# Kernel optimization log

Hardware: AMD Instinct MI355X
Metric: run time of the kernel (lower is better)

## Reference

```python
import jax, jax.numpy as jnp
import numpy as np

D = 2048
H = 16
HD = 128
INNER = H * HD
EPS = 1e-6


def rmsnorm(x, w):
    var = jnp.mean(x * x, axis=-1, keepdims=True)
    return x * jax.lax.rsqrt(var + EPS) * w


def setup_inputs() -> dict:
    key = jax.random.key(0)
    ks = jax.random.split(key, 10)
    B, T, N_ws, T_corr = 2, 2048, 64, 512
    scale = 1.0 / np.sqrt(D)
    return {
        "hidden_states": jax.random.normal(ks[0], (B, T, D), jnp.float32),
        "workspace": jax.random.normal(ks[1], (B, N_ws, D), jnp.float32),
        "correction_tokens": jax.random.normal(ks[2], (B, T_corr, D), jnp.float32),
        "correction_mask": jax.random.randint(ks[3], (B, T_corr), 0, 2, jnp.int32),
        "ln_q_w": jnp.ones((D,), jnp.float32),
        "ln_kv_w": jnp.ones((D,), jnp.float32),
        "Wq": jax.random.normal(ks[4], (D, INNER), jnp.float32) * scale,
        "Wk": jax.random.normal(ks[5], (D, INNER), jnp.float32) * scale,
        "Wv": jax.random.normal(ks[6], (D, INNER), jnp.float32) * scale,
        "Wo": jax.random.normal(ks[7], (INNER, D), jnp.float32) * scale,
    }


def reference(hidden_states, workspace, correction_tokens, correction_mask,
              ln_q_w, ln_kv_w, Wq, Wk, Wv, Wo):
    B, T, _ = hidden_states.shape
    N_ws = workspace.shape[1]
    # kv context = [workspace ; correction_tokens]
    kv_context = jnp.concatenate([workspace, correction_tokens], axis=1)  # (B, N_kv, D)
    N_kv = kv_context.shape[1]
    ws_mask = jnp.ones((B, N_ws), hidden_states.dtype)
    kv_mask = jnp.concatenate([ws_mask, correction_mask.astype(hidden_states.dtype)], axis=1)  # (B, N_kv)

    h = rmsnorm(hidden_states, ln_q_w)
    kv = rmsnorm(kv_context, ln_kv_w)

    q = (h @ Wq).reshape(B, T, H, HD)        # (B,T,H,hd)
    k = (kv @ Wk).reshape(B, N_kv, H, HD)
    v = (kv @ Wv).reshape(B, N_kv, H, HD)

    scores = jnp.einsum("bthd,bshd->bhts", q, k) / np.sqrt(HD)  # (B,H,T,N_kv)
    mask = (kv_mask != 0)[:, None, None, :]                      # (B,1,1,N_kv)
    scores = jnp.where(mask, scores, -jnp.inf)
    attn = jax.nn.softmax(scores, axis=-1)
    attn = jnp.nan_to_num(attn, nan=0.0)
    # dropout is identity in eval mode
    out = jnp.einsum("bhts,bshd->bthd", attn, v).reshape(B, T, INNER)
    return out @ Wo
```

## Files before the change

kernel.cpp:

```cpp
#include <hip/hip_runtime.h>
#include <hip/hip_bf16.h>
#include <math.h>

typedef __bf16 bf16;
typedef __attribute__((ext_vector_type(8))) __bf16 bf16x8;
typedef __attribute__((ext_vector_type(4))) __bf16 bf16x4;
typedef __attribute__((ext_vector_type(4))) float f32x4;

#define D_DIM 2048
#define NKV   576

__device__ inline void gld_lds16(const void* g, void* l) {
    void* gg = const_cast<void*>(g);
    __builtin_amdgcn_global_load_lds(
        (__attribute__((address_space(1))) void*)gg,
        (__attribute__((address_space(3))) void*)l, 16, 0, 0);
}

#define PH_BARRIER() do { __builtin_amdgcn_s_barrier(); asm volatile("" ::: "memory"); } while (0)
#define VMCNT(n)     asm volatile("s_waitcnt vmcnt(" #n ")" ::: "memory")

__global__ __launch_bounds__(256) void prep(
    const float* __restrict__ hidden, const float* __restrict__ wsp,
    const float* __restrict__ corr, const float* __restrict__ lnq,
    const float* __restrict__ lnkv,
    const float* __restrict__ Wq, const float* __restrict__ Wk,
    const float* __restrict__ Wv, const float* __restrict__ Wo,
    bf16* __restrict__ hb, bf16* __restrict__ kvb,
    bf16* __restrict__ WqT, bf16* __restrict__ WkvT, bf16* __restrict__ WoT)
{
    __shared__ float tl[64][65];
    __shared__ float p[4];
    const int id = blockIdx.x, t = threadIdx.x;

    if (id < 4096) {
        const int wz = id >> 10, idx = id & 1023;
        const int wy = idx >> 5, wx = idx & 31;
        const float* in; bf16* out;
        switch (wz) {
            case 0:  in = Wq; out = WqT; break;
            case 1:  in = Wk; out = WkvT; break;
            case 2:  in = Wv; out = WkvT + 2048ull * 2048; break;
            default: in = Wo; out = WoT; break;
        }
        const int r0 = wy * 64, c0 = wx * 64;
        const int tr = t >> 4, tc = (t & 15) * 4;
#pragma unroll
        for (int q = 0; q < 4; ++q) {
            const int r = tr + q * 16;
            float4 v = *(const float4*)(in + (long)(r0 + r) * 2048 + c0 + tc);
            tl[r][tc] = v.x; tl[r][tc + 1] = v.y;
            tl[r][tc + 2] = v.z; tl[r][tc + 3] = v.w;
        }
        __syncthreads();
#pragma unroll
        for (int q = 0; q < 4; ++q) {
            const int orr = tr + q * 16;
            bf16x4 o = { (bf16)tl[tc][orr], (bf16)tl[tc + 1][orr],
                         (bf16)tl[tc + 2][orr], (bf16)tl[tc + 3][orr] };
            *(bf16x4*)(out + (long)(c0 + orr) * 2048 + r0 + tc) = o;
        }
        return;
    }

    const int rr0 = id - 4096;
    const float* xr; const float* w; bf16* yr;
    if (rr0 < 4096) {
        xr = hidden + (long)rr0 * D_DIM; w = lnq; yr = hb + (long)rr0 * D_DIM;
    } else if (rr0 < 4224) {
        const int rr = rr0 - 4096;
        xr = wsp + (long)rr * D_DIM; w = lnkv;
        yr = kvb + ((long)(rr >> 6) * NKV + (rr & 63)) * D_DIM;
    } else {
        const int rr = rr0 - 4224;
        xr = corr + (long)rr * D_DIM; w = lnkv;
        yr = kvb + ((long)(rr >> 9) * NKV + 64 + (rr & 511)) * D_DIM;
    }

    float4 v0 = *(const float4*)(xr + t * 4);
    float4 v1 = *(const float4*)(xr + 1024 + t * 4);
    float ss = v0.x * v0.x + v0.y * v0.y + v0.z * v0.z + v0.w * v0.w
             + v1.x * v1.x + v1.y * v1.y + v1.z * v1.z + v1.w * v1.w;
#pragma unroll
    for (int off = 32; off; off >>= 1) ss += __shfl_xor(ss, off);
    if ((t & 63) == 0) p[t >> 6] = ss;
    __syncthreads();
    const float rs = rsqrtf((p[0] + p[1] + p[2] + p[3]) * (1.0f / 2048.0f) + 1e-6f);

    float4 w0 = *(const float4*)(w + t * 4);
    float4 w1 = *(const float4*)(w + 1024 + t * 4);
    bf16x4 o0 = { (bf16)(v0.x * rs * w0.x), (bf16)(v0.y * rs * w0.y),
                  (bf16)(v0.z * rs * w0.z), (bf16)(v0.w * rs * w0.w) };
    bf16x4 o1 = { (bf16)(v1.x * rs * w1.x), (bf16)(v1.y * rs * w1.y),
                  (bf16)(v1.z * rs * w1.z), (bf16)(v1.w * rs * w1.w) };
    *(bf16x4*)(yr + t * 4) = o0;
    *(bf16x4*)(yr + 1024 + t * 4) = o1;
}

__global__ __launch_bounds__(512, 2) void proj_all(
    const bf16* __restrict__ hb, const bf16* __restrict__ kvb,
    const bf16* __restrict__ WqT, const bf16* __restrict__ WkvT,
    bf16* __restrict__ qb, bf16* __restrict__ kb, bf16* __restrict__ vtb)
{
    __shared__ __align__(16) bf16 smem[4][16384];
    bf16* const EA = smem[0]; bf16* const EB = smem[1];
    bf16* const OA = smem[2]; bf16* const OB = smem[3];

    const int id0 = blockIdx.x;
    const int id = (id0 & 7) * 26 + (id0 >> 3);
    const bf16 *A, *B; int m0, n0; bool isQ;
    if (id < 128) {
        isQ = true;  A = hb;  B = WqT;
        m0 = (id >> 3) * 256; n0 = (id & 7) * 256;
    } else {
        const int kd = id - 128;
        isQ = false; A = kvb; B = WkvT;
        m0 = (kd >> 4) * 256; n0 = (kd & 15) * 256;
    }

    const int tid = threadIdx.x, lane = tid & 63, w = tid >> 6;
    const int wm = (w >> 2) * 128, wn = (w & 3) * 64;
    const int fr = lane & 15, fg = lane >> 4;

    f32x4 acc[8][4] = {};
    bf16x8 af[4][2], bg[4][2];

    const int aoff0 = (wm + fr) * 64 + (fg ^ (fr & 7)) * 8;
    const int boff0 = (wn + fr) * 64 + (fg ^ (fr & 7)) * 8;
    const int aoff1 = aoff0 ^ 32, boff1 = boff0 ^ 32;
    const bf16* const pAE[2] = { EA + aoff0, EA + aoff1 };
    const bf16* const pAO[2] = { OA + aoff0, OA + aoff1 };
    const bf16* const pBE[2] = { EB + boff0, EB + boff1 };
    const bf16* const pBO[2] = { OB + boff0, OB + boff1 };

    const long toff = (long)(tid >> 3) * 2048 + (((tid & 7) ^ ((tid >> 3) & 7)) * 8);
    const bf16* const gA0 = A + (long)m0 * 2048 + toff;
    const bf16* const gA1 = gA0 + 262144;
    const bf16* const gB0 = B + (long)n0 * 2048 + toff;
    const bf16* const gB1 = gB0 + 262144;
    bf16* const dT = (bf16*)smem + tid * 8;

    auto stage2 = [&](const bf16* g, int k, int dslot) {
        gld_lds16(g + k, dT + dslot);
        gld_lds16(g + 131072 + k, dT + dslot + 4096);
    };
    enum { sEA0 = 0, sEA1 = 8192, sEB0 = 16384, sEB1 = 24576,
           sOA0 = 32768, sOA1 = 40960, sOB0 = 49152, sOB1 = 57344 };

    auto load_af = [&](const bf16* const p[2], int ib) {
#pragma unroll
        for (int i = 0; i < 4; ++i)
#pragma unroll
            for (int s = 0; s < 2; ++s)
                af[i][s] = *(const bf16x8*)(p[s] + (ib + i) * 1024);
    };
    auto load_bg4 = [&](const bf16* const p[2]) {
#pragma unroll
        for (int j = 0; j < 4; ++j)
#pragma unroll
            for (int s = 0; s < 2; ++s)
                bg[j][s] = *(const bf16x8*)(p[s] + j * 1024);
    };
    auto mfma16 = [&](int ib, int jb) {
        __builtin_amdgcn_s_setprio(1);
#pragma unroll
        for (int s = 0; s < 2; ++s)
#pragma unroll
            for (int i = 0; i < 4; ++i)
#pragma unroll
                for (int j = 0; j < 2; ++j)
                    acc[ib + i][jb + j] = __builtin_amdgcn_mfma_f32_16x16x32_bf16(
                        af[i][s], bg[jb + j][s], acc[ib + i][jb + j], 0, 0, 0);
        __builtin_amdgcn_s_setprio(0);
    };

    stage2(gA0, 0, sEA0); stage2(gA1, 0, sEA1);
    stage2(gB0, 0, sEB0); stage2(gB1, 0, sEB1);
    stage2(gB0, 64, sOB0); stage2(gB1, 64, sOB1);
    stage2(gA0, 64, sOA0);
    VMCNT(6);
    PH_BARRIER();

    for (int it = 0; it < 15; ++it) {
        const int kO = it * 128 + 64, kE2 = it * 128 + 128, kO2 = it * 128 + 192;
        load_af(pAE, 0); load_bg4(pBE);
        stage2(gA1, kO, sOA1);
        PH_BARRIER(); mfma16(0, 0); PH_BARRIER();
        stage2(gB0, kE2, sEB0);
        PH_BARRIER(); mfma16(0, 2); PH_BARRIER();
        load_af(pAE, 4);
        stage2(gB1, kE2, sEB1);
        PH_BARRIER(); mfma16(4, 2); PH_BARRIER();
        stage2(gA0, kE2, sEA0);
        PH_BARRIER(); mfma16(4, 0); VMCNT(6); PH_BARRIER();
        load_af(pAO, 0); load_bg4(pBO);
        stage2(gA1, kE2, sEA1);
        PH_BARRIER(); mfma16(0, 0); PH_BARRIER();
        stage2(gB0, kO2, sOB0);
        PH_BARRIER(); mfma16(0, 2); PH_BARRIER();
        load_af(pAO, 4);
        stage2(gB1, kO2, sOB1);
        PH_BARRIER(); mfma16(4, 2); PH_BARRIER();
        stage2(gA0, kO2, sOA0);
        PH_BARRIER(); mfma16(4, 0); VMCNT(6); PH_BARRIER();
    }
    {
        load_af(pAE, 0); load_bg4(pBE);
        stage2(gA1, 1984, sOA1);
        PH_BARRIER(); mfma16(0, 0); PH_BARRIER();
        PH_BARRIER(); mfma16(0, 2); PH_BARRIER();
        load_af(pAE, 4);
        PH_BARRIER(); mfma16(4, 2); PH_BARRIER();
        PH_BARRIER(); mfma16(4, 0); VMCNT(0); PH_BARRIER();
        load_af(pAO, 0); load_bg4(pBO);
        PH_BARRIER(); mfma16(0, 0); PH_BARRIER();
        PH_BARRIER(); mfma16(0, 2); PH_BARRIER();
        load_af(pAO, 4);
        PH_BARRIER(); mfma16(4, 2); PH_BARRIER();
        PH_BARRIER(); mfma16(4, 0); PH_BARRIER();
    }

    __syncthreads();

    const int er = fg * 4;
    if (isQ || n0 < 2048) {
        bf16* C = isQ ? qb : kb;
        const int mlim = isQ ? 4096 : 1152;
#pragma unroll
        for (int i = 0; i < 8; ++i)
#pragma unroll
            for (int j = 0; j < 4; ++j) {
                const int n = n0 + wn + j * 16 + fr;
#pragma unroll
                for (int r = 0; r < 4; ++r) {
                    const int m = m0 + wm + i * 16 + er + r;
                    if (m < mlim)
                        C[(long)m * 2048 + n] = (bf16)acc[i][j][r];
                }
            }
        return;
    }

    bf16* T = &smem[0][0];
#pragma unroll
    for (int p2 = 0; p2 < 2; ++p2) {
        if (p2) __syncthreads();
        if ((wn >> 7) == p2) {
            const int nb = wn - p2 * 128;
#pragma unroll
            for (int i = 0; i < 8; ++i)
#pragma unroll
                for (int j = 0; j < 4; ++j) {
                    const int nl = nb + j * 16 + fr;
#pragma unroll
                    for (int r = 0; r < 4; ++r)
                        T[nl * 264 + wm + i * 16 + er + r] = (bf16)acc[i][j][r];
                }
        }
        __syncthreads();
        const int hh = (n0 - 2048 + p2 * 128) >> 7;
        for (int e = tid; e < 128 * 64; e += 512) {
            const int d = e >> 6, mg = (e & 63) * 4;
            const int mm = m0 + mg;
            if (mm < 1152) {
                bf16x4 val = *(const bf16x4*)(T + d * 264 + mg);
                const int bb = mm >= NKV;
                const int s = mm - bb * NKV;
                *(bf16x4*)(vtb + ((long)((bb * 16 + hh) * 128 + d)) * NKV + s) = val;
            }
        }
    }
}

__global__ __launch_bounds__(512, 2) void gemm_final(
    const bf16* __restrict__ Ag, const bf16* __restrict__ Bg, float* __restrict__ C)
{
    __shared__ __align__(16) bf16 smem[49152];
    bf16* const EA = smem;           bf16* const EB = smem + 16384;
    bf16* const OA = smem + 24576;   bf16* const OB = smem + 40960;

    const int id0 = blockIdx.x;
    const int id = (id0 & 7) * 32 + (id0 >> 3);
    const int m0 = (id >> 4) * 256, n0 = (id & 15) * 128;

    const int tid = threadIdx.x, lane = tid & 63, w = tid >> 6;
    const int wm = (w >> 1) * 64, wn = (w & 1) * 64;
    const int fr = lane & 15, fg = lane >> 4;

    f32x4 acc[4][4] = {};
    bf16x8 af[2][2], bg[4][2];

    const int aoff0 = (wm + fr) * 64 + (fg ^ (fr & 7)) * 8;
    const int boff0 = (wn + fr) * 64 + (fg ^ (fr & 7)) * 8;
    const int aoff1 = aoff0 ^ 32, boff1 = boff0 ^ 32;
    const bf16* const pAE[2] = { EA + aoff0, EA + aoff1 };
    const bf16* const pAO[2] = { OA + aoff0, OA + aoff1 };
    const bf16* const pBE[2] = { EB + boff0, EB + boff1 };
    const bf16* const pBO[2] = { OB + boff0, OB + boff1 };

    const long toff = (long)(tid >> 3) * 2048 + (((tid & 7) ^ ((tid >> 3) & 7)) * 8);
    const bf16* const gA0 = Ag + (long)m0 * 2048 + toff;
    const bf16* const gA1 = gA0 + 262144;
    const bf16* const gB0 = Bg + (long)n0 * 2048 + toff;
    bf16* const dT = smem + tid * 8;

    auto stage2 = [&](const bf16* g, int k, int dslot) {
        gld_lds16(g + k, dT + dslot);
        gld_lds16(g + 131072 + k, dT + dslot + 4096);
    };
    enum { sEA0 = 0, sEA1 = 8192, sEB0 = 16384,
           sOA0 = 24576, sOA1 = 32768, sOB0 = 40960 };

    auto load_af = [&](const bf16* const p[2], int ib) {
#pragma unroll
        for (int i = 0; i < 2; ++i)
#pragma unroll
            for (int s = 0; s < 2; ++s)
                af[i][s] = *(const bf16x8*)(p[s] + (ib + i) * 1024);
    };
    auto load_bg4 = [&](const bf16* const p[2]) {
#pragma unroll
        for (int j = 0; j < 4; ++j)
#pragma unroll
            for (int s = 0; s < 2; ++s)
                bg[j][s] = *(const bf16x8*)(p[s] + j * 1024);
    };
    auto mfma8 = [&](int ib, int jb) {
        __builtin_amdgcn_s_setprio(1);
#pragma unroll
        for (int s = 0; s < 2; ++s)
#pragma unroll
            for (int i = 0; i < 2; ++i)
#pragma unroll
                for (int j = 0; j < 2; ++j)
                    acc[ib + i][jb + j] = __builtin_amdgcn_mfma_f32_16x16x32_bf16(
                        af[i][s], bg[jb + j][s], acc[ib + i][jb + j], 0, 0, 0);
        __builtin_amdgcn_s_setprio(0);
    };

    stage2(gA0, 0, sEA0); stage2(gA1, 0, sEA1);
    stage2(gB0, 0, sEB0);
    stage2(gB0, 64, sOB0); stage2(gA0, 64, sOA0);
    VMCNT(4);
    PH_BARRIER();

    for (int it = 0; it < 15; ++it) {
        const int kO = it * 128 + 64, kE2 = it * 128 + 128, kO2 = it * 128 + 192;
        load_af(pAE, 0); load_bg4(pBE);
        stage2(gA1, kO, sOA1);
        PH_BARRIER(); mfma8(0, 0); PH_BARRIER();
        stage2(gB0, kE2, sEB0);
        PH_BARRIER(); mfma8(0, 2); PH_BARRIER();
        load_af(pAE, 2);
        PH_BARRIER(); mfma8(2, 2); PH_BARRIER();
        stage2(gA0, kE2, sEA0);
        PH_BARRIER(); mfma8(2, 0); VMCNT(4); PH_BARRIER();
        load_af(pAO, 0); load_bg4(pBO);
        stage2(gA1, kE2, sEA1);
        PH_BARRIER(); mfma8(0, 0); PH_BARRIER();
        stage2(gB0, kO2, sOB0);
        PH_BARRIER(); mfma8(0, 2); PH_BARRIER();
        load_af(pAO, 2);
        PH_BARRIER(); mfma8(2, 2); PH_BARRIER();
        stage2(gA0, kO2, sOA0);
        PH_BARRIER(); mfma8(2, 0); VMCNT(4); PH_BARRIER();
    }
    {
        load_af(pAE, 0); load_bg4(pBE);
        stage2(gA1, 1984, sOA1);
        PH_BARRIER(); mfma8(0, 0); PH_BARRIER();
        PH_BARRIER(); mfma8(0, 2); PH_BARRIER();
        load_af(pAE, 2);
        PH_BARRIER(); mfma8(2, 2); PH_BARRIER();
        PH_BARRIER(); mfma8(2, 0); VMCNT(0); PH_BARRIER();
        load_af(pAO, 0); load_bg4(pBO);
        PH_BARRIER(); mfma8(0, 0); PH_BARRIER();
        PH_BARRIER(); mfma8(0, 2); PH_BARRIER();
        load_af(pAO, 2);
        PH_BARRIER(); mfma8(2, 2); PH_BARRIER();
        PH_BARRIER(); mfma8(2, 0); PH_BARRIER();
    }

    __syncthreads();

    const int er = fg * 4;
#pragma unroll
    for (int i = 0; i < 4; ++i)
#pragma unroll
        for (int j = 0; j < 4; ++j) {
            const int n = n0 + wn + j * 16 + fr;
#pragma unroll
            for (int r = 0; r < 4; ++r)
                C[(long)(m0 + wm + i * 16 + er + r) * 2048 + n] = acc[i][j][r];
        }
}

__global__ __launch_bounds__(256, 4) void flash_attn(
    const bf16* __restrict__ Q, const bf16* __restrict__ K,
    const bf16* __restrict__ VT, const int* __restrict__ cmask,
    bf16* __restrict__ O)
{
    __shared__ __align__(16) bf16 Ks[64 * 128];
    __shared__ __align__(16) bf16 VTs[128 * 64];

    const int qt = blockIdx.x, h = blockIdx.y, b = blockIdx.z;
    const int tid = threadIdx.x, lane = tid & 63, w = tid >> 6;
    const int fr = lane & 15, fg = lane >> 4;

    const bf16* qbase = Q + ((long)(b * 2048 + qt * 64)) * 2048 + h * 128;
    bf16x8 qf[4];
#pragma unroll
    for (int s = 0; s < 4; ++s)
        qf[s] = *(const bf16x8*)(qbase + (long)(w * 16 + fr) * 2048 + s * 32 + fg * 8);

    float m_r[4], l_r[4];
    f32x4 acc_o[8];
#pragma unroll
    for (int r = 0; r < 4; ++r) { m_r[r] = -3.0e38f; l_r[r] = 0.f; }
#pragma unroll
    for (int j = 0; j < 8; ++j) acc_o[j] = (f32x4){0.f, 0.f, 0.f, 0.f};

    const float scale2 = 0.12752792330124195f;
    const bf16* kbase = K + (long)b * NKV * 2048 + h * 128;
    const bf16* vbase = VT + ((long)(b * 16 + h)) * 128 * NKV;

    for (int kc = 0; kc < 9; ++kc) {
        const int kv0 = kc * 64;
#pragma unroll
        for (int p = 0; p < 4; ++p) {
            const int c = p * 256 + tid;
            const int r = c >> 4, cs = c & 15, cl = cs ^ (r & 15);
            gld_lds16(kbase + (long)(kv0 + r) * 2048 + cl * 8, Ks + c * 8);
        }
#pragma unroll
        for (int p = 0; p < 4; ++p) {
            const int c = p * 256 + tid;
            const int r = c >> 3, cs = c & 7, cl = cs ^ (r & 7);
            gld_lds16(vbase + (long)r * NKV + kv0 + cl * 8, VTs + c * 8);
        }
        __syncthreads();

        f32x4 acc_s[4] = {};
#pragma unroll
        for (int s = 0; s < 4; ++s) {
#pragma unroll
            for (int j = 0; j < 4; ++j) {
                bf16x8 bgv = *(const bf16x8*)(Ks +
                    ((j * 16 + fr) * 16 + ((s * 4 + fg) ^ fr)) * 8);
                acc_s[j] = __builtin_amdgcn_mfma_f32_16x16x32_bf16(qf[s], bgv, acc_s[j], 0, 0, 0);
            }
        }

        float bias[4];
#pragma unroll
        for (int j = 0; j < 4; ++j) {
            const int kv = kv0 + j * 16 + fr;
            const bool valid = (kv < 64) || (cmask[b * 512 + kv - 64] != 0);
            bias[j] = valid ? 0.f : -1e30f;
        }
        float s_f[4][4];
        float mc[4] = {-3.0e38f, -3.0e38f, -3.0e38f, -3.0e38f};
#pragma unroll
        for (int j = 0; j < 4; ++j)
#pragma unroll
            for (int r = 0; r < 4; ++r) {
                float v = fmaf(acc_s[j][r], scale2, bias[j]);
                s_f[j][r] = v; mc[r] = fmaxf(mc[r], v);
            }
#pragma unroll
        for (int r = 0; r < 4; ++r) {
            mc[r] = fmaxf(mc[r], __shfl_xor(mc[r], 1));
            mc[r] = fmaxf(mc[r], __shfl_xor(mc[r], 2));
            mc[r] = fmaxf(mc[r], __shfl_xor(mc[r], 4));
            mc[r] = fmaxf(mc[r], __shfl_xor(mc[r], 8));
        }
        float alpha[4];
#pragma unroll
        for (int r = 0; r < 4; ++r) {
            const float mn = fmaxf(m_r[r], mc[r]);
            alpha[r] = __builtin_amdgcn_exp2f(m_r[r] - mn);
            m_r[r] = mn;
        }
        float rs[4] = {0.f, 0.f, 0.f, 0.f};
#pragma unroll
        for (int j = 0; j < 4; ++j)
#pragma unroll
            for (int r = 0; r < 4; ++r) {
                const float pv = __builtin_amdgcn_exp2f(s_f[j][r] - m_r[r]);
                s_f[j][r] = pv; rs[r] += pv;
            }
#pragma unroll
        for (int r = 0; r < 4; ++r) {
            rs[r] += __shfl_xor(rs[r], 1);
            rs[r] += __shfl_xor(rs[r], 2);
            rs[r] += __shfl_xor(rs[r], 4);
            rs[r] += __shfl_xor(rs[r], 8);
            l_r[r] = l_r[r] * alpha[r] + rs[r];
        }
#pragma unroll
        for (int j = 0; j < 8; ++j)
#pragma unroll
            for (int r = 0; r < 4; ++r) acc_o[j][r] *= alpha[r];

        __syncthreads();

        bf16* Ps = Ks;
#pragma unroll
        for (int j = 0; j < 4; ++j)
#pragma unroll
            for (int r = 0; r < 4; ++r)
                Ps[(w * 16 + fg * 4 + r) * 72 + j * 16 + fr] = (bf16)s_f[j][r];

#pragma unroll
        for (int s2 = 0; s2 < 2; ++s2) {
            bf16x8 afv = *(const bf16x8*)(Ps + (w * 16 + fr) * 72 + s2 * 32 + fg * 8);
#pragma unroll
            for (int jd = 0; jd < 8; ++jd) {
                bf16x8 bgv = *(const bf16x8*)(VTs +
                    ((jd * 16 + fr) * 8 + ((s2 * 4 + fg) ^ (fr & 7))) * 8);
                acc_o[jd] = __builtin_amdgcn_mfma_f32_16x16x32_bf16(afv, bgv, acc_o[jd], 0, 0, 0);
            }
        }
        __syncthreads();
    }

    bf16* obase = O + ((long)(b * 2048 + qt * 64)) * 2048 + h * 128;
#pragma unroll
    for (int r = 0; r < 4; ++r) {
        const float inv = 1.0f / l_r[r];
        const int row = w * 16 + fg * 4 + r;
#pragma unroll
        for (int jd = 0; jd < 8; ++jd)
            obase[(long)row * 2048 + jd * 16 + fr] = (bf16)(acc_o[jd][r] * inv);
    }
}

extern "C" void kernel_launch(void* const* d_in, const int* in_sizes, int n_in,
                              void* d_out, int out_size, void* d_ws, size_t ws_size,
                              hipStream_t stream)
{
    const float* hidden = (const float*)d_in[0];
    const float* wsp    = (const float*)d_in[1];
    const float* corr   = (const float*)d_in[2];
    const int*   cmask  = (const int*)d_in[3];
    const float* lnq    = (const float*)d_in[4];
    const float* lnkv   = (const float*)d_in[5];
    const float* Wq     = (const float*)d_in[6];
    const float* Wk     = (const float*)d_in[7];
    const float* Wv     = (const float*)d_in[8];
    const float* Wo     = (const float*)d_in[9];
    float* out = (float*)d_out;

    char* ws = (char*)d_ws;
    size_t off = 0;
    auto alloc = [&](size_t sz) { void* p = ws + off; off += (sz + 255) & ~(size_t)255; return p; };

    bf16* WqT   = (bf16*)alloc(2048ull * 2048 * 2);
    bf16* WkvT  = (bf16*)alloc(4096ull * 2048 * 2);
    bf16* WoT   = (bf16*)alloc(2048ull * 2048 * 2);
    bf16* hb    = (bf16*)alloc(4096ull * 2048 * 2);
    bf16* kvb   = (bf16*)alloc(1280ull * 2048 * 2);
    bf16* qb    = (bf16*)alloc(4096ull * 2048 * 2);
    bf16* kb    = (bf16*)alloc(1152ull * 2048 * 2);
    bf16* vtb   = (bf16*)alloc(4096ull * NKV * 2);
    bf16* aob   = (bf16*)alloc(4096ull * 2048 * 2);

    prep<<<9344, 256, 0, stream>>>(hidden, wsp, corr, lnq, lnkv,
                                   Wq, Wk, Wv, Wo, hb, kvb, WqT, WkvT, WoT);
    proj_all<<<208, 512, 0, stream>>>(hb, kvb, WqT, WkvT, qb, kb, vtb);
    flash_attn<<<dim3(32, 16, 2), 256, 0, stream>>>(qb, kb, vtb, cmask, aob);
    gemm_final<<<256, 512, 0, stream>>>(aob, WoT, out);
}
```

Measured before the change: 296.6 us.

## Load K/V fragments directly from global memory in attention, drop LDS staging

```diff
diff --git a/kernel.cpp b/kernel.cpp
--- a/kernel.cpp
+++ b/kernel.cpp
@@ -54,11 +54,13 @@
         }
         __syncthreads();
 #pragma unroll
-        for (int q = 0; q < 4; ++q) {
-            const int orr = tr + q * 16;
-            bf16x4 o = { (bf16)tl[tc][orr], (bf16)tl[tc + 1][orr],
-                         (bf16)tl[tc + 2][orr], (bf16)tl[tc + 3][orr] };
-            *(bf16x4*)(out + (long)(c0 + orr) * 2048 + r0 + tc) = o;
+        for (int q = 0; q < 2; ++q) {
+            const int rc = (t >> 3) + q * 32;
+            const int c8 = (t & 7) * 8;
+            bf16x8 o;
+#pragma unroll
+            for (int i = 0; i < 8; ++i) o[i] = (bf16)tl[c8 + i][rc];
+            *(bf16x8*)(out + (long)(c0 + rc) * 2048 + r0 + c8) = o;
         }
         return;
     }
@@ -395,13 +397,12 @@
         }
 }
 
-__global__ __launch_bounds__(256, 4) void flash_attn(
+__global__ __launch_bounds__(256) void flash_attn(
     const bf16* __restrict__ Q, const bf16* __restrict__ K,
     const bf16* __restrict__ VT, const int* __restrict__ cmask,
     bf16* __restrict__ O)
 {
-    __shared__ __align__(16) bf16 Ks[64 * 128];
-    __shared__ __align__(16) bf16 VTs[128 * 64];
+    __shared__ __align__(16) bf16 Ps[64 * 72];
 
     const int qt = blockIdx.x, h = blockIdx.y, b = blockIdx.z;
     const int tid = threadIdx.x, lane = tid & 63, w = tid >> 6;
@@ -421,32 +422,21 @@
     for (int j = 0; j < 8; ++j) acc_o[j] = (f32x4){0.f, 0.f, 0.f, 0.f};
 
     const float scale2 = 0.12752792330124195f;
-    const bf16* kbase = K + (long)b * NKV * 2048 + h * 128;
-    const bf16* vbase = VT + ((long)(b * 16 + h)) * 128 * NKV;
+    const bf16* const kl = K + (long)b * NKV * 2048 + h * 128
+                         + (long)fr * 2048 + fg * 8;
+    const bf16* const vl = VT + ((long)(b * 16 + h)) * 128 * NKV
+                         + (long)fr * NKV + fg * 8;
+    const int* const cm = cmask + b * 512;
 
     for (int kc = 0; kc < 9; ++kc) {
         const int kv0 = kc * 64;
-#pragma unroll
-        for (int p = 0; p < 4; ++p) {
-            const int c = p * 256 + tid;
-            const int r = c >> 4, cs = c & 15, cl = cs ^ (r & 15);
-            gld_lds16(kbase + (long)(kv0 + r) * 2048 + cl * 8, Ks + c * 8);
-        }
-#pragma unroll
-        for (int p = 0; p < 4; ++p) {
-            const int c = p * 256 + tid;
-            const int r = c >> 3, cs = c & 7, cl = cs ^ (r & 7);
-            gld_lds16(vbase + (long)r * NKV + kv0 + cl * 8, VTs + c * 8);
-        }
-        __syncthreads();
 
         f32x4 acc_s[4] = {};
 #pragma unroll
         for (int s = 0; s < 4; ++s) {
 #pragma unroll
             for (int j = 0; j < 4; ++j) {
-                bf16x8 bgv = *(const bf16x8*)(Ks +
-                    ((j * 16 + fr) * 16 + ((s * 4 + fg) ^ fr)) * 8);
+                bf16x8 bgv = *(const bf16x8*)(kl + (long)(kv0 + j * 16) * 2048 + s * 32);
                 acc_s[j] = __builtin_amdgcn_mfma_f32_16x16x32_bf16(qf[s], bgv, acc_s[j], 0, 0, 0);
             }
         }
@@ -455,7 +445,7 @@
 #pragma unroll
         for (int j = 0; j < 4; ++j) {
             const int kv = kv0 + j * 16 + fr;
-            const bool valid = (kv < 64) || (cmask[b * 512 + kv - 64] != 0);
+            const bool valid = (kv < 64) || (cm[kv - 64] != 0);
             bias[j] = valid ? 0.f : -1e30f;
         }
         float s_f[4][4];
@@ -502,9 +492,6 @@
 #pragma unroll
             for (int r = 0; r < 4; ++r) acc_o[j][r] *= alpha[r];
 
-        __syncthreads();
-
-        bf16* Ps = Ks;
 #pragma unroll
         for (int j = 0; j < 4; ++j)
 #pragma unroll
@@ -516,12 +503,10 @@
             bf16x8 afv = *(const bf16x8*)(Ps + (w * 16 + fr) * 72 + s2 * 32 + fg * 8);
 #pragma unroll
             for (int jd = 0; jd < 8; ++jd) {
-                bf16x8 bgv = *(const bf16x8*)(VTs +
-                    ((jd * 16 + fr) * 8 + ((s2 * 4 + fg) ^ (fr & 7))) * 8);
+                bf16x8 bgv = *(const bf16x8*)(vl + (long)(jd * 16) * NKV + kv0 + s2 * 32);
                 acc_o[jd] = __builtin_amdgcn_mfma_f32_16x16x32_bf16(afv, bgv, acc_o[jd], 0, 0, 0);
             }
         }
-        __syncthreads();
     }
 
     bf16* obase = O + ((long)(b * 2048 + qt * 64)) * 2048 + h * 128;
```

Result: slower. 418.9 us (+41.3%).
